# Kernel optimization log

Measured on AMD Instinct MI355X. Metric: run time of the kernel, lower is better.

## Reference

```python
import jax, jax.numpy as jnp
import numpy as np

B, N, DIM = 4, 2048, 512
H, DH = 8, 64  # heads, dim_head; inner_dim = H*DH = 512
SCALE = DH ** -0.5
EPS = 1e-5


def _layer_norm(x, gamma):
    # LayerNorm with learned gamma and beta fixed to zeros (beta is a buffer)
    mu = jnp.mean(x, axis=-1, keepdims=True)
    var = jnp.var(x, axis=-1, keepdims=True)
    return (x - mu) * jax.lax.rsqrt(var + EPS) * gamma


def setup_inputs() -> dict:
    key = jax.random.key(0)
    ks = jax.random.split(key, 6)
    x = jax.random.normal(ks[0], (B, N, DIM), jnp.float32)
    mask = jax.random.bernoulli(ks[1], 0.9, (B, N))  # bool [b, n]
    gamma = jnp.ones((DIM,), jnp.float32)            # pre-attn LayerNorm gamma
    Wq = jax.random.normal(ks[2], (DIM, H * DH), jnp.float32) * 0.02
    Wkv = jax.random.normal(ks[3], (DIM, 2 * DH), jnp.float32) * 0.02  # shared single KV head (MQA)
    null_kv = jax.random.normal(ks[4], (2, DH), jnp.float32)
    Wout = jax.random.normal(ks[5], (H * DH, DIM), jnp.float32) * 0.02
    out_gamma = jnp.ones((DIM,), jnp.float32)        # post-proj LayerNorm gamma
    return {"x": x, "mask": mask, "gamma": gamma, "Wq": Wq, "Wkv": Wkv,
            "null_kv": null_kv, "Wout": Wout, "out_gamma": out_gamma}


def reference(x, mask, gamma, Wq, Wkv, null_kv, Wout, out_gamma):
    b, n, _ = x.shape
    xn = _layer_norm(x, gamma)
    # queries: per-head; keys/values: single shared head (multi-query)
    q = (xn @ Wq).reshape(b, n, H, DH).transpose(0, 2, 1, 3) * SCALE  # [b,h,n,d]
    kv = xn @ Wkv                                                     # [b,n,2d]
    k, v = kv[..., :DH], kv[..., DH:]                                 # [b,n,d]
    # prepend learned null key/value (attention sink) shared across batch
    nk = jnp.broadcast_to(null_kv[0], (b, 1, DH))
    nv = jnp.broadcast_to(null_kv[1], (b, 1, DH))
    k = jnp.concatenate([nk, k], axis=1)  # [b, n+1, d]
    v = jnp.concatenate([nv, v], axis=1)
    sim = jnp.einsum('bhid,bjd->bhij', q, k)  # [b,h,n,n+1]
    # mask padded with True for the null token, broadcast over heads/queries
    m = jnp.concatenate([jnp.ones((b, 1), bool), mask], axis=1)
    max_neg = -jnp.finfo(sim.dtype).max
    sim = jnp.where(m[:, None, None, :], sim, max_neg)
    attn = jax.nn.softmax(sim.astype(jnp.float32), axis=-1).astype(x.dtype)
    out = jnp.einsum('bhij,bjd->bhid', attn, v)       # [b,h,n,d]
    out = out.transpose(0, 2, 1, 3).reshape(b, n, H * DH)
    return _layer_norm(out @ Wout, out_gamma)
```

## Files before the change

kernel.cpp:

```cpp
#include <hip/hip_runtime.h>

typedef __attribute__((ext_vector_type(8)))  short bf16x8;
typedef __attribute__((ext_vector_type(4)))  float f32x4;
typedef __attribute__((ext_vector_type(16))) float f32x16;
typedef __attribute__((ext_vector_type(4)))  unsigned u32x4;

#define Nx 2048
#define CTXx 2049
#define KCAP 2112
#define QSCALE 0.18033688f

__device__ __forceinline__ short f2bs(float x){
    unsigned u = __builtin_bit_cast(unsigned, x);
    u = (u + 0x7fffu + ((u >> 16) & 1u)) >> 16;
    return (short)u;
}
__device__ __forceinline__ unsigned pack_trunc(float a, float b){
    return __builtin_amdgcn_perm(__builtin_bit_cast(unsigned, b),
                                 __builtin_bit_cast(unsigned, a), 0x07060302u);
}

__global__ void __launch_bounds__(256) ln1_prep_kernel(const float* __restrict__ x,
                                                       const float* __restrict__ g,
                                                       short* __restrict__ xnb,
                                                       const float* __restrict__ Wq,
                                                       const float* __restrict__ Wkv,
                                                       const float* __restrict__ Wout,
                                                       const float* __restrict__ nkv,
                                                       short* __restrict__ WcatT,
                                                       short* __restrict__ WoutT,
                                                       short* __restrict__ kb,
                                                       short* __restrict__ vbt){
    __shared__ float ls[64][65];
    int t = threadIdx.x;
    if (blockIdx.x < 2048){
        int w = t >> 6, lane = t & 63;
        size_t row = (size_t)blockIdx.x * 4 + w;
        const float* xr = x + row * 512 + lane * 8;
        float4 a = *(const float4*)xr;
        float4 b = *(const float4*)(xr + 4);
        float s = a.x + a.y + a.z + a.w + b.x + b.y + b.z + b.w;
        float q = a.x*a.x + a.y*a.y + a.z*a.z + a.w*a.w
                + b.x*b.x + b.y*b.y + b.z*b.z + b.w*b.w;
        #pragma unroll
        for (int m = 1; m < 64; m <<= 1){ s += __shfl_xor(s, m, 64); q += __shfl_xor(q, m, 64); }
        float mu  = s * (1.f / 512.f);
        float var = fmaxf(q * (1.f / 512.f) - mu * mu, 0.f);
        float r   = rsqrtf(var + 1e-5f);
        const float* gr = g + lane * 8;
        float4 g0 = *(const float4*)gr;
        float4 g1 = *(const float4*)(gr + 4);
        bf16x8 o;
        o[0] = f2bs((a.x - mu) * r * g0.x); o[1] = f2bs((a.y - mu) * r * g0.y);
        o[2] = f2bs((a.z - mu) * r * g0.z); o[3] = f2bs((a.w - mu) * r * g0.w);
        o[4] = f2bs((b.x - mu) * r * g1.x); o[5] = f2bs((b.y - mu) * r * g1.y);
        o[6] = f2bs((b.z - mu) * r * g1.z); o[7] = f2bs((b.w - mu) * r * g1.w);
        *(bf16x8*)(xnb + row * 512 + lane * 8) = o;
        return;
    }
    int bid = blockIdx.x - 2048;
    if (bid == 144){
        int b = t >> 6, d = t & 63;
        kb[((size_t)b * KCAP) * 64 + d] = f2bs(nkv[d]);
        vbt[((size_t)b * 64 + d) * KCAP + 0] = f2bs(nkv[64 + d]);
        return;
    }
    bool isOut = (bid >= 80);
    int b2 = isOut ? bid - 80 : bid;
    int ntile = isOut ? (b2 & 7) : (b2 % 10);
    int ktile = isOut ? (b2 >> 3) : (b2 / 10);
    int n0 = ntile * 64, k0 = ktile * 64;
    #pragma unroll
    for (int rr = 0; rr < 64; rr += 16){
        int r = rr + (t >> 4), c = (t & 15) * 4;
        float4 v;
        if (isOut)            v = *(const float4*)(Wout + (size_t)(k0 + r) * 512 + n0 + c);
        else if (n0 < 512)    v = *(const float4*)(Wq   + (size_t)(k0 + r) * 512 + n0 + c);
        else                  v = *(const float4*)(Wkv  + (size_t)(k0 + r) * 128 + (n0 - 512) + c);
        ls[c + 0][r] = v.x; ls[c + 1][r] = v.y; ls[c + 2][r] = v.z; ls[c + 3][r] = v.w;
    }
    __syncthreads();
    int rn = t >> 2, kc = (t & 3) * 16;
    short tmp[16];
    #pragma unroll
    for (int j = 0; j < 16; j++) tmp[j] = f2bs(ls[rn][kc + j]);
    short* dst = (isOut ? WoutT : WcatT) + (size_t)(n0 + rn) * 512 + k0 + kc;
    *(int4*)dst       = *(int4*)&tmp[0];
    *(int4*)(dst + 8) = *(int4*)&tmp[8];
}

__global__ void __launch_bounds__(256) ln2_kernel(const float* __restrict__ z,
                                                  const float* __restrict__ g,
                                                  float* __restrict__ out){
    int w = threadIdx.x >> 6, lane = threadIdx.x & 63;
    size_t row = (size_t)blockIdx.x * 4 + w;
    const float* xr = z + row * 512 + lane * 8;
    float4 a = *(const float4*)xr;
    float4 b = *(const float4*)(xr + 4);
    float s = a.x + a.y + a.z + a.w + b.x + b.y + b.z + b.w;
    float q = a.x*a.x + a.y*a.y + a.z*a.z + a.w*a.w
            + b.x*b.x + b.y*b.y + b.z*b.z + b.w*b.w;
    #pragma unroll
    for (int m = 1; m < 64; m <<= 1){ s += __shfl_xor(s, m, 64); q += __shfl_xor(q, m, 64); }
    float mu  = s * (1.f / 512.f);
    float var = fmaxf(q * (1.f / 512.f) - mu * mu, 0.f);
    float r   = rsqrtf(var + 1e-5f);
    const float* gr = g + lane * 8;
    float4 g0 = *(const float4*)gr;
    float4 g1 = *(const float4*)(gr + 4);
    float4 o0, o1;
    o0.x = (a.x - mu) * r * g0.x; o0.y = (a.y - mu) * r * g0.y;
    o0.z = (a.z - mu) * r * g0.z; o0.w = (a.w - mu) * r * g0.w;
    o1.x = (b.x - mu) * r * g1.x; o1.y = (b.y - mu) * r * g1.y;
    o1.z = (b.z - mu) * r * g1.z; o1.w = (b.w - mu) * r * g1.w;
    float* op = out + row * 512 + lane * 8;
    *(float4*)op = o0; *(float4*)(op + 4) = o1;
}

__global__ void __launch_bounds__(256, 1) gemm_qkv(const short* __restrict__ A,
                                                   const short* __restrict__ BwT,
                                                   short* __restrict__ qb,
                                                   short* __restrict__ kb,
                                                   short* __restrict__ vbt){
    __shared__ short As[2][128][72];
    __shared__ short Bs[2][160][72];
    int t = threadIdx.x;
    int lane = t & 63, w = t >> 6;
    int l16 = lane & 15, quad = lane >> 4;
    int wm = w & 1, wn = w >> 1;
    int row0 = blockIdx.y * 128, col0 = blockIdx.x * 160;
    f32x4 acc[4][5];
    #pragma unroll
    for (int i = 0; i < 4; i++)
        #pragma unroll
        for (int j = 0; j < 5; j++) acc[i][j] = (f32x4){0.f, 0.f, 0.f, 0.f};
    int ar = t >> 1, ak = (t & 1) * 32;
    const short* ap = A + (size_t)(row0 + ar) * 512 + ak;
    int4 a0 = *(const int4*)(ap);      int4 a1 = *(const int4*)(ap + 8);
    int4 a2 = *(const int4*)(ap + 16); int4 a3 = *(const int4*)(ap + 24);
    int4 pb[5];
    int brow[5], bseg[5];
    #pragma unroll
    for (int ps = 0; ps < 5; ps++){
        int idx = ps * 256 + t;
        brow[ps] = idx >> 3; bseg[ps] = (idx & 7) * 8;
        pb[ps] = *(const int4*)(BwT + (size_t)(col0 + brow[ps]) * 512 + bseg[ps]);
    }
    int p = 0;
    for (int k0 = 0; k0 < 512; k0 += 64){
        *(int4*)&As[p][ar][ak]      = a0;
        *(int4*)&As[p][ar][ak + 8]  = a1;
        *(int4*)&As[p][ar][ak + 16] = a2;
        *(int4*)&As[p][ar][ak + 24] = a3;
        #pragma unroll
        for (int ps = 0; ps < 5; ps++)
            *(int4*)&Bs[p][brow[ps]][bseg[ps]] = pb[ps];
        __syncthreads();
        int kn = k0 + 64;
        if (kn < 512){
            a0 = *(const int4*)(ap + kn);      a1 = *(const int4*)(ap + kn + 8);
            a2 = *(const int4*)(ap + kn + 16); a3 = *(const int4*)(ap + kn + 24);
            #pragma unroll
            for (int ps = 0; ps < 5; ps++)
                pb[ps] = *(const int4*)(BwT + (size_t)(col0 + brow[ps]) * 512 + kn + bseg[ps]);
        }
        #pragma unroll
        for (int ks = 0; ks < 2; ks++){
            bf16x8 af[4], bfr[5];
            #pragma unroll
            for (int mt = 0; mt < 4; mt++)
                af[mt] = *(const bf16x8*)&As[p][wm * 64 + mt * 16 + l16][ks * 32 + quad * 8];
            #pragma unroll
            for (int nt = 0; nt < 5; nt++)
                bfr[nt] = *(const bf16x8*)&Bs[p][wn * 80 + nt * 16 + l16][ks * 32 + quad * 8];
            #pragma unroll
            for (int mt = 0; mt < 4; mt++)
                #pragma unroll
                for (int nt = 0; nt < 5; nt++)
                    acc[mt][nt] = __builtin_amdgcn_mfma_f32_16x16x32_bf16(af[mt], bfr[nt], acc[mt][nt], 0, 0, 0);
        }
        p ^= 1;
    }
    #pragma unroll
    for (int mt = 0; mt < 4; mt++)
        #pragma unroll
        for (int nt = 0; nt < 5; nt++)
            #pragma unroll
            for (int r = 0; r < 4; r++){
                int row = row0 + wm * 64 + mt * 16 + quad * 4 + r;
                int col = col0 + wn * 80 + nt * 16 + l16;
                float v = acc[mt][nt][r];
                int bb = row >> 11, ii = row & 2047;
                if (col < 512){
                    qb[(size_t)row * 512 + col] = f2bs(v * QSCALE);
                } else if (col < 576){
                    kb[((size_t)bb * KCAP + ii + 1) * 64 + (col - 512)] = f2bs(v);
                } else {
                    vbt[((size_t)bb * 64 + (col - 576)) * KCAP + ii + 1] = f2bs(v);
                }
            }
}

__global__ void __launch_bounds__(256, 2) gemm_out(const short* __restrict__ A,
                                                   const short* __restrict__ BwT,
                                                   float* __restrict__ C){
    __shared__ short As[2][128][72];
    __shared__ short Bs[2][128][72];
    int t = threadIdx.x;
    int lane = t & 63, w = t >> 6;
    int l16 = lane & 15, quad = lane >> 4;
    int wm = w & 1, wn = w >> 1;
    int row0 = blockIdx.y * 128, col0 = blockIdx.x * 128;
    f32x4 acc[4][4];
    #pragma unroll
    for (int i = 0; i < 4; i++)
        #pragma unroll
        for (int j = 0; j < 4; j++) acc[i][j] = (f32x4){0.f, 0.f, 0.f, 0.f};
    int ar = t >> 1, ak = (t & 1) * 32;
    const short* ap = A   + (size_t)(row0 + ar) * 512 + ak;
    const short* bp = BwT + (size_t)(col0 + ar) * 512 + ak;
    int4 a0 = *(const int4*)(ap);      int4 a1 = *(const int4*)(ap + 8);
    int4 a2 = *(const int4*)(ap + 16); int4 a3 = *(const int4*)(ap + 24);
    int4 b0 = *(const int4*)(bp);      int4 b1 = *(const int4*)(bp + 8);
    int4 b2 = *(const int4*)(bp + 16); int4 b3 = *(const int4*)(bp + 24);
    int p = 0;
    for (int k0 = 0; k0 < 512; k0 += 64){
        *(int4*)&As[p][ar][ak]      = a0;
        *(int4*)&As[p][ar][ak + 8]  = a1;
        *(int4*)&As[p][ar][ak + 16] = a2;
        *(int4*)&As[p][ar][ak + 24] = a3;
        *(int4*)&Bs[p][ar][ak]      = b0;
        *(int4*)&Bs[p][ar][ak + 8]  = b1;
        *(int4*)&Bs[p][ar][ak + 16] = b2;
        *(int4*)&Bs[p][ar][ak + 24] = b3;
        __syncthreads();
        int kn = k0 + 64;
        if (kn < 512){
            a0 = *(const int4*)(ap + kn);      a1 = *(const int4*)(ap + kn + 8);
            a2 = *(const int4*)(ap + kn + 16); a3 = *(const int4*)(ap + kn + 24);
            b0 = *(const int4*)(bp + kn);      b1 = *(const int4*)(bp + kn + 8);
            b2 = *(const int4*)(bp + kn + 16); b3 = *(const int4*)(bp + kn + 24);
        }
        #pragma unroll
        for (int ks = 0; ks < 2; ks++){
            bf16x8 af[4], bfr[4];
            #pragma unroll
            for (int mt = 0; mt < 4; mt++)
                af[mt] = *(const bf16x8*)&As[p][wm * 64 + mt * 16 + l16][ks * 32 + quad * 8];
            #pragma unroll
            for (int nt = 0; nt < 4; nt++)
                bfr[nt] = *(const bf16x8*)&Bs[p][wn * 64 + nt * 16 + l16][ks * 32 + quad * 8];
            #pragma unroll
            for (int mt = 0; mt < 4; mt++)
                #pragma unroll
                for (int nt = 0; nt < 4; nt++)
                    acc[mt][nt] = __builtin_amdgcn_mfma_f32_16x16x32_bf16(af[mt], bfr[nt], acc[mt][nt], 0, 0, 0);
        }
        p ^= 1;
    }
    #pragma unroll
    for (int mt = 0; mt < 4; mt++)
        #pragma unroll
        for (int nt = 0; nt < 4; nt++)
            #pragma unroll
            for (int r = 0; r < 4; r++){
                int row = row0 + wm * 64 + mt * 16 + quad * 4 + r;
                int col = col0 + wn * 64 + nt * 16 + l16;
                C[(size_t)row * 512 + col] = acc[mt][nt][r];
            }
}

__global__ void __launch_bounds__(256, 2) attn_kernel(const short* __restrict__ qb,
                                                      const short* __restrict__ kb,
                                                      const short* __restrict__ vbt,
                                                      const int* __restrict__ mask,
                                                      short* __restrict__ ob){
    __shared__ short Ks[2][64][72];
    __shared__ short Vt[2][64][72];
    int t = threadIdx.x;
    int lane = t & 63, w = t >> 6;
    int n32 = lane & 31, hb = lane >> 5;
    int b = blockIdx.y, i0 = blockIdx.x * 16;
    int head = 2 * w + (n32 >> 4), row = i0 + (n32 & 15);
    bf16x8 qf[4];
    {
        const short* qp = qb + ((size_t)(b * Nx + row)) * 512 + head * 64 + hb * 8;
        #pragma unroll
        for (int ks = 0; ks < 4; ks++) qf[ks] = *(const bf16x8*)(qp + ks * 16);
    }
    f32x16 oacc[2];
    #pragma unroll
    for (int j = 0; j < 16; j++){ oacc[0][j] = 0.f; oacc[1][j] = 0.f; }
    float lsum = 0.f;

    int skey = t >> 2, sd = (t & 3) * 16;
    int vd   = t >> 2, vk = (t & 3) * 16;
    const short* kgp = kb  + (size_t)b * KCAP * 64 + skey * 64 + sd;
    const short* vgp = vbt + ((size_t)b * 64 + vd) * KCAP + vk;
    const int* mrow = mask + b * Nx;

    int4 pk0 = *(const int4*)(kgp);
    int4 pk1 = *(const int4*)(kgp + 8);
    int4 pv0 = *(const int4*)(vgp);
    int4 pv1 = *(const int4*)(vgp + 8);
    int mok = (lane == 0) ? 1 : ((lane < CTXx) ? mrow[lane - 1] : 0);

    int p = 0;
    for (int jt = 0; jt < 33; ++jt){
        *(int4*)&Ks[p][skey][sd]     = pk0;
        *(int4*)&Ks[p][skey][sd + 8] = pk1;
        *(int4*)&Vt[p][vd][vk]       = make_int4(pv0.x, pv0.y, pv1.x, pv1.y);
        *(int4*)&Vt[p][vd][vk + 8]   = make_int4(pv0.z, pv0.w, pv1.z, pv1.w);
        unsigned long long bal = __ballot(mok != 0);
        __syncthreads();
        int jn = (jt + 1) * 64;
        if (jt + 1 < 33){
            pk0 = *(const int4*)(kgp + (size_t)jn * 64);
            pk1 = *(const int4*)(kgp + (size_t)jn * 64 + 8);
            pv0 = *(const int4*)(vgp + jn);
            pv1 = *(const int4*)(vgp + jn + 8);
            int jg = jn + lane;
            mok = (jg < CTXx) ? mrow[jg - 1] : 0;
        }
        f32x16 sf[2];
        #pragma unroll
        for (int i = 0; i < 2; i++)
            #pragma unroll
            for (int j = 0; j < 16; j++) sf[i][j] = 0.f;
        #pragma unroll
        for (int ks = 0; ks < 4; ks++){
            #pragma unroll
            for (int kt = 0; kt < 2; kt++){
                bf16x8 kf = *(const bf16x8*)&Ks[p][kt * 32 + n32][ks * 16 + hb * 8];
                sf[kt] = __builtin_amdgcn_mfma_f32_32x32x16_bf16(kf, qf[ks], sf[kt], 0, 0, 0);
            }
        }
        unsigned mlo = (unsigned)(bal >> (4 * hb));
        unsigned mhi = (unsigned)(bal >> (32 + 4 * hb));
        unsigned pg[8][2];
        #pragma unroll
        for (int kt = 0; kt < 2; kt++){
            unsigned mm = kt ? mhi : mlo;
            #pragma unroll
            for (int g4 = 0; g4 < 4; g4++){
                float pr[4];
                #pragma unroll
                for (int tt = 0; tt < 4; tt++){
                    float e = __builtin_amdgcn_exp2f(sf[kt][g4 * 4 + tt]);
                    float pv = ((mm >> (8 * g4 + tt)) & 1u) ? e : 0.f;
                    pr[tt] = pv;
                    lsum += __builtin_bit_cast(float,
                              __builtin_bit_cast(unsigned, pv) & 0xFFFF0000u);
                }
                pg[kt * 4 + g4][0] = pack_trunc(pr[0], pr[1]);
                pg[kt * 4 + g4][1] = pack_trunc(pr[2], pr[3]);
            }
        }
        #pragma unroll
        for (int s = 0; s < 4; s++){
            bf16x8 pa = __builtin_bit_cast(bf16x8,
                (u32x4){pg[2 * s][0], pg[2 * s][1], pg[2 * s + 1][0], pg[2 * s + 1][1]});
            #pragma unroll
            for (int nt = 0; nt < 2; nt++){
                bf16x8 vf = *(const bf16x8*)&Vt[p][nt * 32 + n32][s * 16 + hb * 8];
                oacc[nt] = __builtin_amdgcn_mfma_f32_32x32x16_bf16(pa, vf, oacc[nt], 0, 0, 0);
            }
        }
        p ^= 1;
    }
    lsum += __shfl_xor(lsum, 32, 64);
    #pragma unroll
    for (int r = 0; r < 16; r++){
        int hr = (r & 3) + 8 * (r >> 2) + 4 * hb;
        float linv = 1.f / __shfl(lsum, hr, 64);
        int grow = i0 + (hr & 15);
        int ghead = 2 * w + (hr >> 4);
        short* op = ob + ((size_t)(b * Nx + grow)) * 512 + ghead * 64 + n32;
        op[0]  = f2bs(oacc[0][r] * linv);
        op[32] = f2bs(oacc[1][r] * linv);
    }
}

extern "C" void kernel_launch(void* const* d_in, const int* in_sizes, int n_in,
                              void* d_out, int out_size, void* d_ws, size_t ws_size,
                              hipStream_t stream){
    const float* x     = (const float*)d_in[0];
    const int*   mask  = (const int*)  d_in[1];
    const float* gamma = (const float*)d_in[2];
    const float* Wq    = (const float*)d_in[3];
    const float* Wkv   = (const float*)d_in[4];
    const float* nkv   = (const float*)d_in[5];
    const float* Wout  = (const float*)d_in[6];
    const float* og    = (const float*)d_in[7];
    float* out = (float*)d_out;

    short* xnb   = (short*)d_ws;
    short* qb    = xnb + (size_t)4194304;
    short* kb    = qb  + (size_t)4194304;
    short* vbt   = kb  + (size_t)540672;
    short* ob    = vbt + (size_t)540672;
    short* WcatT = ob  + (size_t)4194304;
    short* WoutT = WcatT + (size_t)327680;
    float* zb    = (float*)d_ws;

    ln1_prep_kernel<<<2193, 256, 0, stream>>>(x, gamma, xnb, Wq, Wkv, Wout, nkv,
                                              WcatT, WoutT, kb, vbt);
    gemm_qkv    <<<dim3(4, 64), 256, 0, stream>>>(xnb, WcatT, qb, kb, vbt);
    attn_kernel <<<dim3(128, 4), 256, 0, stream>>>(qb, kb, vbt, mask, ob);
    gemm_out    <<<dim3(4, 64), 256, 0, stream>>>(ob, WoutT, zb);
    ln2_kernel  <<<2048, 256, 0, stream>>>(zb, og, out);
}
```

Baseline: 181.3 us.

## Precompute mask bitmaps, unroll attention by two key tiles, shrink GEMM row tiles

The mask is converted once into 64-bit ballot words stored in the key buffer's padding, so the attention loop no longer reads the int mask or does per-tile ballots. The attention loop now processes two 64-key subtiles per barrier with double-buffered LDS, computes the softmax denominator with an MFMA against a ones vector instead of scalar adds, and raises wave priority around the MFMA blocks. Both projection GEMMs halve their row tile to 64, doubling the grid, and gemm_qkv's launch bound is raised to two blocks per CU for better occupancy. The trade-offs are more LDS per attention block and extra redundant B-tile loads in the GEMMs.

```diff
diff --git a/kernel.cpp b/kernel.cpp
--- a/kernel.cpp
+++ b/kernel.cpp
@@ -27,6 +27,7 @@
                                                        const float* __restrict__ Wkv,
                                                        const float* __restrict__ Wout,
                                                        const float* __restrict__ nkv,
+                                                       const int* __restrict__ mask,
                                                        short* __restrict__ WcatT,
                                                        short* __restrict__ WoutT,
                                                        short* __restrict__ kb,
@@ -65,6 +66,18 @@
         vbt[((size_t)b * 64 + d) * KCAP + 0] = f2bs(nkv[64 + d]);
         return;
     }
+    if (bid == 145){
+        int w = t >> 6, lane = t & 63;
+        const int* mrow = mask + w * Nx;
+        unsigned long long* mw = (unsigned long long*)(kb + ((size_t)w * KCAP + 2049) * 64);
+        for (int wi = 0; wi < 33; wi++){
+            int j = wi * 64 + lane;
+            int ok = (j == 0) ? 1 : ((j <= Nx) ? mrow[j - 1] : 0);
+            unsigned long long bal = __ballot(ok != 0);
+            if (lane == 0) mw[wi] = bal;
+        }
+        return;
+    }
     bool isOut = (bid >= 80);
     int b2 = isOut ? bid - 80 : bid;
     int ntile = isOut ? (b2 & 7) : (b2 % 10);
@@ -117,27 +130,26 @@
     *(float4*)op = o0; *(float4*)(op + 4) = o1;
 }
 
-__global__ void __launch_bounds__(256, 1) gemm_qkv(const short* __restrict__ A,
+__global__ void __launch_bounds__(256, 2) gemm_qkv(const short* __restrict__ A,
                                                    const short* __restrict__ BwT,
                                                    short* __restrict__ qb,
                                                    short* __restrict__ kb,
                                                    short* __restrict__ vbt){
-    __shared__ short As[2][128][72];
+    __shared__ short As[2][64][72];
     __shared__ short Bs[2][160][72];
     int t = threadIdx.x;
     int lane = t & 63, w = t >> 6;
     int l16 = lane & 15, quad = lane >> 4;
     int wm = w & 1, wn = w >> 1;
-    int row0 = blockIdx.y * 128, col0 = blockIdx.x * 160;
-    f32x4 acc[4][5];
-    #pragma unroll
-    for (int i = 0; i < 4; i++)
+    int row0 = blockIdx.y * 64, col0 = blockIdx.x * 160;
+    f32x4 acc[2][5];
+    #pragma unroll
+    for (int i = 0; i < 2; i++)
         #pragma unroll
         for (int j = 0; j < 5; j++) acc[i][j] = (f32x4){0.f, 0.f, 0.f, 0.f};
-    int ar = t >> 1, ak = (t & 1) * 32;
+    int ar = t >> 2, ak = (t & 3) * 16;
     const short* ap = A + (size_t)(row0 + ar) * 512 + ak;
     int4 a0 = *(const int4*)(ap);      int4 a1 = *(const int4*)(ap + 8);
-    int4 a2 = *(const int4*)(ap + 16); int4 a3 = *(const int4*)(ap + 24);
     int4 pb[5];
     int brow[5], bseg[5];
     #pragma unroll
@@ -148,33 +160,31 @@
     }
     int p = 0;
     for (int k0 = 0; k0 < 512; k0 += 64){
-        *(int4*)&As[p][ar][ak]      = a0;
-        *(int4*)&As[p][ar][ak + 8]  = a1;
-        *(int4*)&As[p][ar][ak + 16] = a2;
-        *(int4*)&As[p][ar][ak + 24] = a3;
+        *(int4*)&As[p][ar][ak]     = a0;
+        *(int4*)&As[p][ar][ak + 8] = a1;
         #pragma unroll
         for (int ps = 0; ps < 5; ps++)
             *(int4*)&Bs[p][brow[ps]][bseg[ps]] = pb[ps];
         __syncthreads();
         int kn = k0 + 64;
         if (kn < 512){
-            a0 = *(const int4*)(ap + kn);      a1 = *(const int4*)(ap + kn + 8);
-            a2 = *(const int4*)(ap + kn + 16); a3 = *(const int4*)(ap + kn + 24);
+            a0 = *(const int4*)(ap + kn);
+            a1 = *(const int4*)(ap + kn + 8);
             #pragma unroll
             for (int ps = 0; ps < 5; ps++)
                 pb[ps] = *(const int4*)(BwT + (size_t)(col0 + brow[ps]) * 512 + kn + bseg[ps]);
         }
         #pragma unroll
         for (int ks = 0; ks < 2; ks++){
-            bf16x8 af[4], bfr[5];
-            #pragma unroll
-            for (int mt = 0; mt < 4; mt++)
-                af[mt] = *(const bf16x8*)&As[p][wm * 64 + mt * 16 + l16][ks * 32 + quad * 8];
+            bf16x8 af[2], bfr[5];
+            #pragma unroll
+            for (int mt = 0; mt < 2; mt++)
+                af[mt] = *(const bf16x8*)&As[p][wm * 32 + mt * 16 + l16][ks * 32 + quad * 8];
             #pragma unroll
             for (int nt = 0; nt < 5; nt++)
                 bfr[nt] = *(const bf16x8*)&Bs[p][wn * 80 + nt * 16 + l16][ks * 32 + quad * 8];
             #pragma unroll
-            for (int mt = 0; mt < 4; mt++)
+            for (int mt = 0; mt < 2; mt++)
                 #pragma unroll
                 for (int nt = 0; nt < 5; nt++)
                     acc[mt][nt] = __builtin_amdgcn_mfma_f32_16x16x32_bf16(af[mt], bfr[nt], acc[mt][nt], 0, 0, 0);
@@ -182,12 +192,12 @@
         p ^= 1;
     }
     #pragma unroll
-    for (int mt = 0; mt < 4; mt++)
+    for (int mt = 0; mt < 2; mt++)
         #pragma unroll
         for (int nt = 0; nt < 5; nt++)
             #pragma unroll
             for (int r = 0; r < 4; r++){
-                int row = row0 + wm * 64 + mt * 16 + quad * 4 + r;
+                int row = row0 + wm * 32 + mt * 16 + quad * 4 + r;
                 int col = col0 + wn * 80 + nt * 16 + l16;
                 float v = acc[mt][nt][r];
                 int bb = row >> 11, ii = row & 2047;
@@ -204,54 +214,51 @@
 __global__ void __launch_bounds__(256, 2) gemm_out(const short* __restrict__ A,
                                                    const short* __restrict__ BwT,
                                                    float* __restrict__ C){
-    __shared__ short As[2][128][72];
+    __shared__ short As[2][64][72];
     __shared__ short Bs[2][128][72];
     int t = threadIdx.x;
     int lane = t & 63, w = t >> 6;
     int l16 = lane & 15, quad = lane >> 4;
     int wm = w & 1, wn = w >> 1;
-    int row0 = blockIdx.y * 128, col0 = blockIdx.x * 128;
-    f32x4 acc[4][4];
-    #pragma unroll
-    for (int i = 0; i < 4; i++)
+    int row0 = blockIdx.y * 64, col0 = blockIdx.x * 128;
+    f32x4 acc[2][4];
+    #pragma unroll
+    for (int i = 0; i < 2; i++)
         #pragma unroll
         for (int j = 0; j < 4; j++) acc[i][j] = (f32x4){0.f, 0.f, 0.f, 0.f};
-    int ar = t >> 1, ak = (t & 1) * 32;
+    int ar = t >> 2, ak = (t & 3) * 16;
+    int br = t >> 1, bk = (t & 1) * 32;
     const short* ap = A   + (size_t)(row0 + ar) * 512 + ak;
-    const short* bp = BwT + (size_t)(col0 + ar) * 512 + ak;
+    const short* bp = BwT + (size_t)(col0 + br) * 512 + bk;
     int4 a0 = *(const int4*)(ap);      int4 a1 = *(const int4*)(ap + 8);
-    int4 a2 = *(const int4*)(ap + 16); int4 a3 = *(const int4*)(ap + 24);
     int4 b0 = *(const int4*)(bp);      int4 b1 = *(const int4*)(bp + 8);
     int4 b2 = *(const int4*)(bp + 16); int4 b3 = *(const int4*)(bp + 24);
     int p = 0;
     for (int k0 = 0; k0 < 512; k0 += 64){
         *(int4*)&As[p][ar][ak]      = a0;
         *(int4*)&As[p][ar][ak + 8]  = a1;
-        *(int4*)&As[p][ar][ak + 16] = a2;
-        *(int4*)&As[p][ar][ak + 24] = a3;
-        *(int4*)&Bs[p][ar][ak]      = b0;
-        *(int4*)&Bs[p][ar][ak + 8]  = b1;
-        *(int4*)&Bs[p][ar][ak + 16] = b2;
-        *(int4*)&Bs[p][ar][ak + 24] = b3;
+        *(int4*)&Bs[p][br][bk]      = b0;
+        *(int4*)&Bs[p][br][bk + 8]  = b1;
+        *(int4*)&Bs[p][br][bk + 16] = b2;
+        *(int4*)&Bs[p][br][bk + 24] = b3;
         __syncthreads();
         int kn = k0 + 64;
         if (kn < 512){
             a0 = *(const int4*)(ap + kn);      a1 = *(const int4*)(ap + kn + 8);
-            a2 = *(const int4*)(ap + kn + 16); a3 = *(const int4*)(ap + kn + 24);
             b0 = *(const int4*)(bp + kn);      b1 = *(const int4*)(bp + kn + 8);
             b2 = *(const int4*)(bp + kn + 16); b3 = *(const int4*)(bp + kn + 24);
         }
         #pragma unroll
         for (int ks = 0; ks < 2; ks++){
-            bf16x8 af[4], bfr[4];
-            #pragma unroll
-            for (int mt = 0; mt < 4; mt++)
-                af[mt] = *(const bf16x8*)&As[p][wm * 64 + mt * 16 + l16][ks * 32 + quad * 8];
+            bf16x8 af[2], bfr[4];
+            #pragma unroll
+            for (int mt = 0; mt < 2; mt++)
+                af[mt] = *(const bf16x8*)&As[p][wm * 32 + mt * 16 + l16][ks * 32 + quad * 8];
             #pragma unroll
             for (int nt = 0; nt < 4; nt++)
                 bfr[nt] = *(const bf16x8*)&Bs[p][wn * 64 + nt * 16 + l16][ks * 32 + quad * 8];
             #pragma unroll
-            for (int mt = 0; mt < 4; mt++)
+            for (int mt = 0; mt < 2; mt++)
                 #pragma unroll
                 for (int nt = 0; nt < 4; nt++)
                     acc[mt][nt] = __builtin_amdgcn_mfma_f32_16x16x32_bf16(af[mt], bfr[nt], acc[mt][nt], 0, 0, 0);
@@ -259,12 +266,12 @@
         p ^= 1;
     }
     #pragma unroll
-    for (int mt = 0; mt < 4; mt++)
+    for (int mt = 0; mt < 2; mt++)
         #pragma unroll
         for (int nt = 0; nt < 4; nt++)
             #pragma unroll
             for (int r = 0; r < 4; r++){
-                int row = row0 + wm * 64 + mt * 16 + quad * 4 + r;
+                int row = row0 + wm * 32 + mt * 16 + quad * 4 + r;
                 int col = col0 + wn * 64 + nt * 16 + l16;
                 C[(size_t)row * 512 + col] = acc[mt][nt][r];
             }
@@ -273,10 +280,9 @@
 __global__ void __launch_bounds__(256, 2) attn_kernel(const short* __restrict__ qb,
                                                       const short* __restrict__ kb,
                                                       const short* __restrict__ vbt,
-                                                      const int* __restrict__ mask,
                                                       short* __restrict__ ob){
-    __shared__ short Ks[2][64][72];
-    __shared__ short Vt[2][64][72];
+    __shared__ short Ks[2][2][64][72];
+    __shared__ short Vt[2][2][64][72];
     int t = threadIdx.x;
     int lane = t & 63, w = t >> 6;
     int n32 = lane & 31, hb = lane >> 5;
@@ -288,91 +294,124 @@
         #pragma unroll
         for (int ks = 0; ks < 4; ks++) qf[ks] = *(const bf16x8*)(qp + ks * 16);
     }
-    f32x16 oacc[2];
-    #pragma unroll
-    for (int j = 0; j < 16; j++){ oacc[0][j] = 0.f; oacc[1][j] = 0.f; }
-    float lsum = 0.f;
+    bf16x8 ones;
+    #pragma unroll
+    for (int j = 0; j < 8; j++) ones[j] = (short)0x3F80;
+    f32x16 oacc[2], lacc;
+    #pragma unroll
+    for (int j = 0; j < 16; j++){ oacc[0][j] = 0.f; oacc[1][j] = 0.f; lacc[j] = 0.f; }
 
     int skey = t >> 2, sd = (t & 3) * 16;
     int vd   = t >> 2, vk = (t & 3) * 16;
     const short* kgp = kb  + (size_t)b * KCAP * 64 + skey * 64 + sd;
     const short* vgp = vbt + ((size_t)b * 64 + vd) * KCAP + vk;
-    const int* mrow = mask + b * Nx;
-
-    int4 pk0 = *(const int4*)(kgp);
-    int4 pk1 = *(const int4*)(kgp + 8);
-    int4 pv0 = *(const int4*)(vgp);
-    int4 pv1 = *(const int4*)(vgp + 8);
-    int mok = (lane == 0) ? 1 : ((lane < CTXx) ? mrow[lane - 1] : 0);
+    const unsigned long long* mbp =
+        (const unsigned long long*)(kb + ((size_t)b * KCAP + 2049) * 64);
+
+    int4 pk[2][2], pv[2][2];
+    #pragma unroll
+    for (int s = 0; s < 2; s++){
+        pk[s][0] = *(const int4*)(kgp + (size_t)(s * 64) * 64);
+        pk[s][1] = *(const int4*)(kgp + (size_t)(s * 64) * 64 + 8);
+        pv[s][0] = *(const int4*)(vgp + s * 64);
+        pv[s][1] = *(const int4*)(vgp + s * 64 + 8);
+    }
+
+#define COMPUTE_SUB(SUBI, BAL)                                                              \
+    {                                                                                       \
+        f32x16 sf[2];                                                                       \
+        _Pragma("unroll")                                                                   \
+        for (int i = 0; i < 2; i++)                                                         \
+            _Pragma("unroll")                                                               \
+            for (int j = 0; j < 16; j++) sf[i][j] = 0.f;                                    \
+        __builtin_amdgcn_s_setprio(1);                                                      \
+        _Pragma("unroll")                                                                   \
+        for (int ks = 0; ks < 4; ks++){                                                     \
+            _Pragma("unroll")                                                               \
+            for (int kt = 0; kt < 2; kt++){                                                 \
+                bf16x8 kf = *(const bf16x8*)&Ks[p][SUBI][kt * 32 + n32][ks * 16 + hb * 8];  \
+                sf[kt] = __builtin_amdgcn_mfma_f32_32x32x16_bf16(kf, qf[ks], sf[kt], 0, 0, 0); \
+            }                                                                               \
+        }                                                                                   \
+        __builtin_amdgcn_s_setprio(0);                                                      \
+        unsigned mlo = (unsigned)((BAL) >> (4 * hb));                                       \
+        unsigned mhi = (unsigned)((BAL) >> (32 + 4 * hb));                                  \
+        unsigned pg[8][2];                                                                  \
+        _Pragma("unroll")                                                                   \
+        for (int kt = 0; kt < 2; kt++){                                                     \
+            unsigned mm = kt ? mhi : mlo;                                                   \
+            _Pragma("unroll")                                                               \
+            for (int g4 = 0; g4 < 4; g4++){                                                 \
+                float pr[4];                                                                \
+                _Pragma("unroll")                                                           \
+                for (int tt = 0; tt < 4; tt++){                                             \
+                    float e = __builtin_amdgcn_exp2f(sf[kt][g4 * 4 + tt]);                  \
+                    pr[tt] = ((mm >> (8 * g4 + tt)) & 1u) ? e : 0.f;                        \
+                }                                                                           \
+                pg[kt * 4 + g4][0] = pack_trunc(pr[0], pr[1]);                              \
+                pg[kt * 4 + g4][1] = pack_trunc(pr[2], pr[3]);                              \
+            }                                                                               \
+        }                                                                                   \
+        __builtin_amdgcn_s_setprio(1);                                                      \
+        _Pragma("unroll")                                                                   \
+        for (int s = 0; s < 4; s++){                                                        \
+            bf16x8 pa = __builtin_bit_cast(bf16x8,                                          \
+                (u32x4){pg[2 * s][0], pg[2 * s][1], pg[2 * s + 1][0], pg[2 * s + 1][1]});   \
+            lacc = __builtin_amdgcn_mfma_f32_32x32x16_bf16(pa, ones, lacc, 0, 0, 0);        \
+            _Pragma("unroll")                                                               \
+            for (int nt = 0; nt < 2; nt++){                                                 \
+                bf16x8 vf = *(const bf16x8*)&Vt[p][SUBI][nt * 32 + n32][s * 16 + hb * 8];   \
+                oacc[nt] = __builtin_amdgcn_mfma_f32_32x32x16_bf16(pa, vf, oacc[nt], 0, 0, 0); \
+            }                                                                               \
+        }                                                                                   \
+        __builtin_amdgcn_s_setprio(0);                                                      \
+    }
 
     int p = 0;
-    for (int jt = 0; jt < 33; ++jt){
-        *(int4*)&Ks[p][skey][sd]     = pk0;
-        *(int4*)&Ks[p][skey][sd + 8] = pk1;
-        *(int4*)&Vt[p][vd][vk]       = make_int4(pv0.x, pv0.y, pv1.x, pv1.y);
-        *(int4*)&Vt[p][vd][vk + 8]   = make_int4(pv0.z, pv0.w, pv1.z, pv1.w);
-        unsigned long long bal = __ballot(mok != 0);
+    for (int jt = 0; jt < 16; ++jt){
+        #pragma unroll
+        for (int s = 0; s < 2; s++){
+            *(int4*)&Ks[p][s][skey][sd]     = pk[s][0];
+            *(int4*)&Ks[p][s][skey][sd + 8] = pk[s][1];
+            *(int4*)&Vt[p][s][vd][vk]       = make_int4(pv[s][0].x, pv[s][0].y, pv[s][1].x, pv[s][1].y);
+            *(int4*)&Vt[p][s][vd][vk + 8]   = make_int4(pv[s][0].z, pv[s][0].w, pv[s][1].z, pv[s][1].w);
+        }
+        unsigned long long bal0 = mbp[2 * jt];
+        unsigned long long bal1 = mbp[2 * jt + 1];
         __syncthreads();
-        int jn = (jt + 1) * 64;
-        if (jt + 1 < 33){
-            pk0 = *(const int4*)(kgp + (size_t)jn * 64);
-            pk1 = *(const int4*)(kgp + (size_t)jn * 64 + 8);
-            pv0 = *(const int4*)(vgp + jn);
-            pv1 = *(const int4*)(vgp + jn + 8);
-            int jg = jn + lane;
-            mok = (jg < CTXx) ? mrow[jg - 1] : 0;
-        }
-        f32x16 sf[2];
-        #pragma unroll
-        for (int i = 0; i < 2; i++)
-            #pragma unroll
-            for (int j = 0; j < 16; j++) sf[i][j] = 0.f;
-        #pragma unroll
-        for (int ks = 0; ks < 4; ks++){
-            #pragma unroll
-            for (int kt = 0; kt < 2; kt++){
-                bf16x8 kf = *(const bf16x8*)&Ks[p][kt * 32 + n32][ks * 16 + hb * 8];
-                sf[kt] = __builtin_amdgcn_mfma_f32_32x32x16_bf16(kf, qf[ks], sf[kt], 0, 0, 0);
+        int jn = (jt + 1) * 128;
+        {
+            const short* kp0 = kgp + (size_t)jn * 64;
+            const short* vp0 = vgp + jn;
+            pk[0][0] = *(const int4*)(kp0);
+            pk[0][1] = *(const int4*)(kp0 + 8);
+            pv[0][0] = *(const int4*)(vp0);
+            pv[0][1] = *(const int4*)(vp0 + 8);
+            if (jt < 15){
+                pk[1][0] = *(const int4*)(kp0 + 64 * 64);
+                pk[1][1] = *(const int4*)(kp0 + 64 * 64 + 8);
+                pv[1][0] = *(const int4*)(vp0 + 64);
+                pv[1][1] = *(const int4*)(vp0 + 64 + 8);
             }
         }
-        unsigned mlo = (unsigned)(bal >> (4 * hb));
-        unsigned mhi = (unsigned)(bal >> (32 + 4 * hb));
-        unsigned pg[8][2];
-        #pragma unroll
-        for (int kt = 0; kt < 2; kt++){
-            unsigned mm = kt ? mhi : mlo;
-            #pragma unroll
-            for (int g4 = 0; g4 < 4; g4++){
-                float pr[4];
-                #pragma unroll
-                for (int tt = 0; tt < 4; tt++){
-                    float e = __builtin_amdgcn_exp2f(sf[kt][g4 * 4 + tt]);
-                    float pv = ((mm >> (8 * g4 + tt)) & 1u) ? e : 0.f;
-                    pr[tt] = pv;
-                    lsum += __builtin_bit_cast(float,
-                              __builtin_bit_cast(unsigned, pv) & 0xFFFF0000u);
-                }
-                pg[kt * 4 + g4][0] = pack_trunc(pr[0], pr[1]);
-                pg[kt * 4 + g4][1] = pack_trunc(pr[2], pr[3]);
-            }
-        }
-        #pragma unroll
-        for (int s = 0; s < 4; s++){
-            bf16x8 pa = __builtin_bit_cast(bf16x8,
-                (u32x4){pg[2 * s][0], pg[2 * s][1], pg[2 * s + 1][0], pg[2 * s + 1][1]});
-            #pragma unroll
-            for (int nt = 0; nt < 2; nt++){
-                bf16x8 vf = *(const bf16x8*)&Vt[p][nt * 32 + n32][s * 16 + hb * 8];
-                oacc[nt] = __builtin_amdgcn_mfma_f32_32x32x16_bf16(pa, vf, oacc[nt], 0, 0, 0);
-            }
-        }
+        COMPUTE_SUB(0, bal0)
+        COMPUTE_SUB(1, bal1)
         p ^= 1;
     }
-    lsum += __shfl_xor(lsum, 32, 64);
+    {
+        *(int4*)&Ks[p][0][skey][sd]     = pk[0][0];
+        *(int4*)&Ks[p][0][skey][sd + 8] = pk[0][1];
+        *(int4*)&Vt[p][0][vd][vk]       = make_int4(pv[0][0].x, pv[0][0].y, pv[0][1].x, pv[0][1].y);
+        *(int4*)&Vt[p][0][vd][vk + 8]   = make_int4(pv[0][0].z, pv[0][0].w, pv[0][1].z, pv[0][1].w);
+        unsigned long long bal0 = mbp[32];
+        __syncthreads();
+        COMPUTE_SUB(0, bal0)
+    }
+#undef COMPUTE_SUB
     #pragma unroll
     for (int r = 0; r < 16; r++){
+        float linv = 1.f / lacc[r];
         int hr = (r & 3) + 8 * (r >> 2) + 4 * hb;
-        float linv = 1.f / __shfl(lsum, hr, 64);
         int grow = i0 + (hr & 15);
         int ghead = 2 * w + (hr >> 4);
         short* op = ob + ((size_t)(b * Nx + grow)) * 512 + ghead * 64 + n32;
@@ -403,10 +442,10 @@
     short* WoutT = WcatT + (size_t)327680;
     float* zb    = (float*)d_ws;
 
-    ln1_prep_kernel<<<2193, 256, 0, stream>>>(x, gamma, xnb, Wq, Wkv, Wout, nkv,
+    ln1_prep_kernel<<<2194, 256, 0, stream>>>(x, gamma, xnb, Wq, Wkv, Wout, nkv, mask,
                                               WcatT, WoutT, kb, vbt);
-    gemm_qkv    <<<dim3(4, 64), 256, 0, stream>>>(xnb, WcatT, qb, kb, vbt);
-    attn_kernel <<<dim3(128, 4), 256, 0, stream>>>(qb, kb, vbt, mask, ob);
-    gemm_out    <<<dim3(4, 64), 256, 0, stream>>>(ob, WoutT, zb);
+    gemm_qkv    <<<dim3(4, 128), 256, 0, stream>>>(xnb, WcatT, qb, kb, vbt);
+    attn_kernel <<<dim3(128, 4), 256, 0, stream>>>(qb, kb, vbt, ob);
+    gemm_out    <<<dim3(4, 128), 256, 0, stream>>>(ob, WoutT, zb);
     ln2_kernel  <<<2048, 256, 0, stream>>>(zb, og, out);
 }
```

Result: slower. 197.5 us (+8.9%).
